# Optimization experiments

Hardware: AMD Instinct MI355X
Metric: run time of the kernel (lower is better)

The kernel has to match this reference:

```python
import jax, jax.numpy as jnp
import numpy as np

NUM_ITERATIONS = 4
STEP = 1
N_NODES = 50000
N_EDGES = 800000
D_FEAT = 64


def setup_inputs() -> dict:
    key = jax.random.key(0)
    k1, k2, k3 = jax.random.split(key, 3)
    x = jax.random.normal(k1, (N_NODES, D_FEAT), dtype=jnp.float32)
    src = jax.random.randint(k2, (N_EDGES,), 0, N_NODES, dtype=jnp.int64)
    dst = jax.random.randint(k3, (N_EDGES,), 0, N_NODES, dtype=jnp.int64)
    edge_index = jnp.stack([src, dst], axis=0)
    return {"x": x, "edge_index": edge_index}


def _wl_conv(x, src, dst, n_nodes):
    # continuous WL: x_i' = 0.5 * (x_i + mean_{j in N(i)} x_j)
    msg = x[src]  # [E, D] gather of neighbor features
    summed = jax.ops.segment_sum(msg, dst, num_segments=n_nodes)  # [N, D]
    deg = jax.ops.segment_sum(jnp.ones_like(dst, dtype=x.dtype), dst,
                              num_segments=n_nodes)  # [N]
    mean = summed / jnp.maximum(deg, 1.0)[:, None]  # isolated nodes -> 0
    return 0.5 * (x + mean)


def reference(x, edge_index):
    n_nodes = x.shape[0]
    src, dst = edge_index[0], edge_index[1]
    feats = [x]
    for _ in range(NUM_ITERATIONS):
        for _ in range(STEP):
            x = _wl_conv(x, src, dst, n_nodes)
        feats.append(x)
    return jnp.concatenate(feats, axis=-1)  # [N, (num_iterations+1)*D]
```

## Files before the change

### kernel.cpp

```cpp
#include <hip/hip_runtime.h>

constexpr int N = 50000;
constexpr int E = 800000;
constexpr int D = 64;
constexpr int DOUT = 320;
constexpr int CAPD = 64;
constexpr int NBUCK = (N + 255) / 256;
constexpr int SLAB = 5120;
constexpr int PART_BLOCKS = 256;
constexpr int CONV_BLOCKS = (N * 16 + 255) / 256;
constexpr int ITER_BLOCKS = 2048;
constexpr int SCAN_BLOCKS = (N + 255) / 256;

__device__ __forceinline__ unsigned short f2bf(float f) {
    unsigned int u = __float_as_uint(f);
    unsigned int r = (u + 0x7fffu + ((u >> 16) & 1u)) >> 16;
    return (unsigned short)r;
}
__device__ __forceinline__ unsigned int pack2(float a, float b) {
    return (unsigned int)f2bf(a) | ((unsigned int)f2bf(b) << 16);
}
__device__ __forceinline__ float bflo(unsigned int u) { return __uint_as_float(u << 16); }
__device__ __forceinline__ float bfhi(unsigned int u) { return __uint_as_float(u & 0xFFFF0000u); }

__global__ __launch_bounds__(256) void part_conv_kernel(
    const int* __restrict__ ei32,
    const float* __restrict__ x,
    float* __restrict__ out,
    unsigned int* __restrict__ mirror,
    int* __restrict__ cursor,
    unsigned int* __restrict__ slab) {
    if (blockIdx.x >= PART_BLOCKS) {
        int i = (blockIdx.x - PART_BLOCKS) * 256 + threadIdx.x;
        if (i < N * 16) {
            int n = i >> 4, j = i & 15;
            float4 v = ((const float4*)x)[i];
            ((float4*)(out + (size_t)n * DOUT))[j] = v;
            uint2 m = make_uint2(pack2(v.x, v.y), pack2(v.z, v.w));
            ((uint2*)(mirror + (size_t)n * 32))[j] = m;
        }
        return;
    }
    __shared__ int hcnt[NBUCK];
    __shared__ int hbase[NBUCK];
    int t = threadIdx.x;
    for (int k = t; k < NBUCK; k += 256) hcnt[k] = 0;
    int lane = t & 63;
    int wv = ei32[2 * lane + 1];
    int is64 = (__ballot(wv != 0) == 0ULL) ? 1 : 0;
    __syncthreads();

    const int EPB = E / PART_BLOCKS;
    int i0 = blockIdx.x * EPB;
    for (int k = t; k < EPB; k += 256) {
        int i = i0 + k;
        int d = is64 ? ei32[2 * (E + i)] : ei32[E + i];
        atomicAdd(&hcnt[d >> 8], 1);
    }
    __syncthreads();
    for (int k = t; k < NBUCK; k += 256) {
        hbase[k] = atomicAdd(&cursor[k], hcnt[k]);
        hcnt[k] = 0;
    }
    __syncthreads();
    for (int k = t; k < EPB; k += 256) {
        int i = i0 + k;
        int s = is64 ? ei32[2 * i] : ei32[i];
        int d = is64 ? ei32[2 * (E + i)] : ei32[E + i];
        int b = d >> 8;
        int r = atomicAdd(&hcnt[b], 1);
        int p = hbase[b] + r;
        if (p < SLAB)
            slab[(size_t)b * SLAB + p] = (unsigned int)s | ((unsigned int)(d & 255) << 16);
    }
}

__global__ __launch_bounds__(256) void lds_build_kernel(
    const unsigned int* __restrict__ slab,
    const int* __restrict__ cursor,
    int* __restrict__ cnt,
    unsigned short* __restrict__ csr) {
    __shared__ unsigned short rows[256 * CAPD];
    __shared__ int lcnt[256];
    int b = blockIdx.x;
    int t = threadIdx.x;
    lcnt[t] = 0;
    __syncthreads();
    int sz = min(cursor[b], SLAB);
    const unsigned int* sp = slab + (size_t)b * SLAB;
    for (int k = t; k < sz; k += 256) {
        unsigned int rec = sp[k];
        int dlo = (rec >> 16) & 255;
        int r = atomicAdd(&lcnt[dlo], 1);
        if (r < CAPD) rows[dlo * CAPD + r] = (unsigned short)(rec & 0xFFFFu);
    }
    __syncthreads();
    int node = b * 256 + t;
    if (node < N) cnt[node] = min(lcnt[t], CAPD);
    for (int k = t; k < 256 * (CAPD / 8); k += 256) {
        int nd = k >> 3;
        int j = k & 7;
        int g = b * 256 + nd;
        if (g < N && j * 8 < lcnt[nd]) {
            *(uint4*)(csr + (size_t)g * CAPD + j * 8) =
                *(const uint4*)(rows + nd * CAPD + j * 8);
        }
    }
}


__global__ __launch_bounds__(256) void wl_iter_bf16_kernel(
    const unsigned int* __restrict__ min_,
    unsigned int* __restrict__ mout,
    const float* __restrict__ self_in,
    float* __restrict__ xout,
    const int* __restrict__ cnt, const unsigned short* __restrict__ csr) {
    int gw = blockIdx.x * 4 + (threadIdx.x >> 6);
    int lane = threadIdx.x & 63;
    int g = lane >> 3;
    int fi = lane & 7;
    const int NW = ITER_BLOCKS * 4;

    int deg_cur = (gw < N) ? min(cnt[gw], CAPD) : 0;
    for (int w = gw; w < N; w += NW) {
        int wn = w + NW;
        int deg_nxt = (wn < N) ? min(cnt[wn], CAPD) : 0;
        int deg = deg_cur;
        size_t base = (size_t)w * CAPD;

        float a[8], b[8];
#pragma unroll
        for (int k = 0; k < 8; ++k) { a[k] = 0.f; b[k] = 0.f; }

#define ACC8(u, arr)                                                     \
        arr[0] += bflo(u.x); arr[1] += bfhi(u.x);                        \
        arr[2] += bflo(u.y); arr[3] += bfhi(u.y);                        \
        arr[4] += bflo(u.z); arr[5] += bfhi(u.z);                        \
        arr[6] += bflo(u.w); arr[7] += bfhi(u.w);

        int e = g;
        for (; e + 8 < deg; e += 16) {
            int s0 = csr[base + e], s1 = csr[base + e + 8];
            uint4 u0 = *(const uint4*)(min_ + (size_t)s0 * 32 + fi * 4);
            uint4 u1 = *(const uint4*)(min_ + (size_t)s1 * 32 + fi * 4);
            ACC8(u0, a); ACC8(u1, b);
        }
        if (e < deg) {
            int s = csr[base + e];
            uint4 u = *(const uint4*)(min_ + (size_t)s * 32 + fi * 4);
            ACC8(u, a);
        }
#undef ACC8
#pragma unroll
        for (int k = 0; k < 8; ++k) {
            a[k] += b[k];
            a[k] += __shfl_xor(a[k], 8);
            a[k] += __shfl_xor(a[k], 16);
            a[k] += __shfl_xor(a[k], 32);
        }
        float inv = (deg > 0) ? 0.5f / (float)deg : 0.0f;
        if (g == 0) {
            const float* srow = self_in + (size_t)w * DOUT + fi * 8;
            float4 s0 = *(const float4*)(srow);
            float4 s1 = *(const float4*)(srow + 4);
            float r0 = 0.5f * s0.x + inv * a[0];
            float r1 = 0.5f * s0.y + inv * a[1];
            float r2 = 0.5f * s0.z + inv * a[2];
            float r3 = 0.5f * s0.w + inv * a[3];
            float r4 = 0.5f * s1.x + inv * a[4];
            float r5 = 0.5f * s1.y + inv * a[5];
            float r6 = 0.5f * s1.z + inv * a[6];
            float r7 = 0.5f * s1.w + inv * a[7];
            float* drow = xout + (size_t)w * DOUT + fi * 8;
            *(float4*)(drow)     = make_float4(r0, r1, r2, r3);
            *(float4*)(drow + 4) = make_float4(r4, r5, r6, r7);
            if (mout) {
                uint4 m = make_uint4(pack2(r0, r1), pack2(r2, r3),
                                     pack2(r4, r5), pack2(r6, r7));
                *(uint4*)(mout + (size_t)w * 32 + fi * 4) = m;
            }
        }
        deg_cur = deg_nxt;
    }
}


__global__ void detect_kernel(const int* __restrict__ ei32, int* __restrict__ flag) {
    if (blockIdx.x == 0 && threadIdx.x == 0) {
        int s = 0;
        for (int k = 0; k < 128; ++k) s |= ei32[2 * k + 1];
        *flag = (s == 0) ? 1 : 0;
    }
}
__device__ __forceinline__ int load_src(const int* ei32, int is64, int i) {
    return is64 ? ei32[2 * i] : ei32[i];
}
__device__ __forceinline__ int load_dst(const int* ei32, int is64, int i) {
    return is64 ? ei32[2 * (E + i)] : ei32[E + i];
}

__global__ __launch_bounds__(256) void hist_kernel(const int* __restrict__ ei32,
                                                   const int* __restrict__ flag,
                                                   int* __restrict__ cnt) {
    int i = blockIdx.x * 256 + threadIdx.x;
    int is64 = *flag;
    if (i < E) atomicAdd(&cnt[load_dst(ei32, is64, i)], 1);
}

__global__ __launch_bounds__(256) void scan1_kernel(const int* __restrict__ cnt,
                                                    int* __restrict__ offs,
                                                    int* __restrict__ P) {
    __shared__ int sm[256];
    int t = threadIdx.x;
    int i = blockIdx.x * 256 + t;
    int v = (i < N) ? cnt[i] : 0;
    sm[t] = v; __syncthreads();
    for (int o = 1; o < 256; o <<= 1) {
        int u = (t >= o) ? sm[t - o] : 0;
        __syncthreads();
        sm[t] += u;
        __syncthreads();
    }
    if (i < N) offs[i] = sm[t] - v;
    if (t == 255) P[blockIdx.x] = sm[255];
}

__global__ __launch_bounds__(256) void scan2_kernel(int* __restrict__ P,
                                                    int* __restrict__ offs) {
    __shared__ int sm[256];
    int t = threadIdx.x;
    int v = (t < SCAN_BLOCKS) ? P[t] : 0;
    sm[t] = v; __syncthreads();
    for (int o = 1; o < 256; o <<= 1) {
        int u = (t >= o) ? sm[t - o] : 0;
        __syncthreads();
        sm[t] += u;
        __syncthreads();
    }
    if (t < SCAN_BLOCKS) P[t] = sm[t] - v;
    if (t == 255) offs[N] = sm[255];
}

__global__ __launch_bounds__(256) void scan3_kernel(int* __restrict__ offs,
                                                    const int* __restrict__ P) {
    int i = blockIdx.x * 256 + threadIdx.x;
    if (i < N) offs[i] += P[blockIdx.x];
}

__global__ __launch_bounds__(256) void scatter_kernel(const int* __restrict__ ei32,
                                                      const int* __restrict__ flag,
                                                      const int* __restrict__ offs,
                                                      int* __restrict__ cursor,
                                                      int* __restrict__ csr) {
    int i = blockIdx.x * 256 + threadIdx.x;
    int is64 = *flag;
    if (i < E) {
        int d = load_dst(ei32, is64, i);
        int p = atomicAdd(&cursor[d], 1);
        csr[offs[d] + p] = load_src(ei32, is64, i);
    }
}

__global__ __launch_bounds__(256) void chunk0_kernel(const float* __restrict__ x,
                                                     float* __restrict__ out) {
    int i = blockIdx.x * 256 + threadIdx.x;
    if (i < N * 16) {
        int n = i >> 4, j = i & 15;
        float4 v = ((const float4*)x)[i];
        ((float4*)(out + (size_t)n * DOUT))[j] = v;
    }
}

__global__ __launch_bounds__(256) void wl_iter_kernel(
    const float* __restrict__ xin, float* __restrict__ xout,
    const int* __restrict__ offs, const int* __restrict__ csr) {
    int w = blockIdx.x * 4 + (threadIdx.x >> 6);
    if (w >= N) return;
    int lane = threadIdx.x & 63;
    int g = lane >> 4, fi = lane & 15;
    int beg = offs[w], end = offs[w + 1];
    float4 a0 = make_float4(0.f, 0.f, 0.f, 0.f);
    float4 a1 = make_float4(0.f, 0.f, 0.f, 0.f);
    int e = beg + g;
    for (; e + 4 < end; e += 8) {
        int s0 = csr[e], s1 = csr[e + 4];
        float4 v0 = *(const float4*)(xin + (size_t)s0 * DOUT + fi * 4);
        float4 v1 = *(const float4*)(xin + (size_t)s1 * DOUT + fi * 4);
        a0.x += v0.x; a0.y += v0.y; a0.z += v0.z; a0.w += v0.w;
        a1.x += v1.x; a1.y += v1.y; a1.z += v1.z; a1.w += v1.w;
    }
    if (e < end) {
        int s = csr[e];
        float4 v = *(const float4*)(xin + (size_t)s * DOUT + fi * 4);
        a0.x += v.x; a0.y += v.y; a0.z += v.z; a0.w += v.w;
    }
    float4 acc;
    acc.x = a0.x + a1.x; acc.y = a0.y + a1.y;
    acc.z = a0.z + a1.z; acc.w = a0.w + a1.w;
    acc.x += __shfl_xor(acc.x, 16); acc.y += __shfl_xor(acc.y, 16);
    acc.z += __shfl_xor(acc.z, 16); acc.w += __shfl_xor(acc.w, 16);
    acc.x += __shfl_xor(acc.x, 32); acc.y += __shfl_xor(acc.y, 32);
    acc.z += __shfl_xor(acc.z, 32); acc.w += __shfl_xor(acc.w, 32);
    int deg = end - beg;
    float inv = (deg > 0) ? 0.5f / (float)deg : 0.0f;
    if (g == 0) {
        float4 s4 = *(const float4*)(xin + (size_t)w * DOUT + fi * 4);
        float4 r;
        r.x = 0.5f * s4.x + inv * acc.x;
        r.y = 0.5f * s4.y + inv * acc.y;
        r.z = 0.5f * s4.z + inv * acc.z;
        r.w = 0.5f * s4.w + inv * acc.w;
        *(float4*)(xout + (size_t)w * DOUT + fi * 4) = r;
    }
}


extern "C" void kernel_launch(void* const* d_in, const int* in_sizes, int n_in,
                              void* d_out, int out_size, void* d_ws, size_t ws_size,
                              hipStream_t stream) {
    const float* x  = (const float*)d_in[0];
    const int* ei32 = (const int*)d_in[1];
    float* out = (float*)d_out;

    int* cursor = (int*)d_ws;
    int* cnt = cursor + 256;
    unsigned int* slab = (unsigned int*)(cnt + N);
    unsigned short* csr = (unsigned short*)(slab + (size_t)NBUCK * SLAB);
    unsigned int* mirA = (unsigned int*)((char*)csr + (size_t)N * CAPD * 2);
    unsigned int* mirB = mirA + (size_t)N * 32;
    size_t need = 256 * 4 + (size_t)N * 4 + (size_t)NBUCK * SLAB * 4 +
                  (size_t)N * CAPD * 2 + (size_t)2 * N * 32 * 4;

    dim3 b256(256);
    dim3 gE((E + 255) / 256);
    dim3 gIter(ITER_BLOCKS);
    dim3 gConv((N * 16 + 255) / 256);

    if (ws_size >= need) {
        hipMemsetAsync(cursor, 0, 256 * sizeof(int), stream);
        part_conv_kernel<<<dim3(PART_BLOCKS + CONV_BLOCKS), b256, 0, stream>>>(
            ei32, x, out, mirA, cursor, slab);
        lds_build_kernel<<<dim3(NBUCK), b256, 0, stream>>>(slab, cursor, cnt, csr);
        wl_iter_bf16_kernel<<<gIter, b256, 0, stream>>>(
            mirA, mirB, out + 0 * D, out + 1 * D, cnt, csr);
        wl_iter_bf16_kernel<<<gIter, b256, 0, stream>>>(
            mirB, mirA, out + 1 * D, out + 2 * D, cnt, csr);
        wl_iter_bf16_kernel<<<gIter, b256, 0, stream>>>(
            mirA, mirB, out + 2 * D, out + 3 * D, cnt, csr);
        wl_iter_bf16_kernel<<<gIter, b256, 0, stream>>>(
            mirB, (unsigned int*)nullptr, out + 3 * D, out + 4 * D, cnt, csr);
    } else {
        int* flag  = (int*)d_ws;
        int* fcnt  = flag + 16;
        int* foffs = fcnt + N;
        int* P     = foffs + (N + 1);
        int* fcsr  = P + 256;
        detect_kernel<<<1, 64, 0, stream>>>(ei32, flag);
        hipMemsetAsync(fcnt, 0, (size_t)N * 4, stream);
        hist_kernel<<<gE, b256, 0, stream>>>(ei32, flag, fcnt);
        scan1_kernel<<<dim3(SCAN_BLOCKS), b256, 0, stream>>>(fcnt, foffs, P);
        scan2_kernel<<<1, b256, 0, stream>>>(P, foffs);
        scan3_kernel<<<dim3(SCAN_BLOCKS), b256, 0, stream>>>(foffs, P);
        hipMemsetAsync(fcnt, 0, (size_t)N * 4, stream);
        scatter_kernel<<<gE, b256, 0, stream>>>(ei32, flag, foffs, fcnt, fcsr);
        chunk0_kernel<<<gConv, b256, 0, stream>>>(x, out);
        for (int c = 1; c <= 4; ++c) {
            wl_iter_kernel<<<dim3((N + 3) / 4), b256, 0, stream>>>(
                out + (size_t)(c - 1) * D, out + (size_t)c * D, foffs, fcsr);
        }
    }
}
```

Before: 204.1 us.

## Process two nodes per wave, issue neighbor loads early, widen build and partition grids

Each wave in the iteration kernel now handles two adjacent nodes at once. It issues the self-row loads and the first 16 neighbor gathers of both nodes up front, then runs an interleaved loop over both nodes' remaining neighbors. This raises memory-level parallelism on the latency-bound bf16 gathers. The grid is resized to 3125 blocks so each wave does exactly one pair. The LDS CSR build now uses 512 threads per block, and the partition kernel uses more blocks; both are meant to improve occupancy during preprocessing. The cost is more registers, which may lower occupancy, and divergence when the two nodes have different degrees.

```diff
diff --git a/kernel.cpp b/kernel.cpp
--- a/kernel.cpp
+++ b/kernel.cpp
@@ -7,9 +7,9 @@
 constexpr int CAPD = 64;
 constexpr int NBUCK = (N + 255) / 256;
 constexpr int SLAB = 5120;
-constexpr int PART_BLOCKS = 256;
+constexpr int PART_BLOCKS = 400;
 constexpr int CONV_BLOCKS = (N * 16 + 255) / 256;
-constexpr int ITER_BLOCKS = 2048;
+constexpr int ITER_BLOCKS = 3125;
 constexpr int SCAN_BLOCKS = (N + 255) / 256;
 
 __device__ __forceinline__ unsigned short f2bf(float f) {
@@ -75,7 +75,7 @@
     }
 }
 
-__global__ __launch_bounds__(256) void lds_build_kernel(
+__global__ __launch_bounds__(512) void lds_build_kernel(
     const unsigned int* __restrict__ slab,
     const int* __restrict__ cursor,
     int* __restrict__ cnt,
@@ -84,11 +84,11 @@
     __shared__ int lcnt[256];
     int b = blockIdx.x;
     int t = threadIdx.x;
-    lcnt[t] = 0;
+    if (t < 256) lcnt[t] = 0;
     __syncthreads();
     int sz = min(cursor[b], SLAB);
     const unsigned int* sp = slab + (size_t)b * SLAB;
-    for (int k = t; k < sz; k += 256) {
+    for (int k = t; k < sz; k += 512) {
         unsigned int rec = sp[k];
         int dlo = (rec >> 16) & 255;
         int r = atomicAdd(&lcnt[dlo], 1);
@@ -96,8 +96,8 @@
     }
     __syncthreads();
     int node = b * 256 + t;
-    if (node < N) cnt[node] = min(lcnt[t], CAPD);
-    for (int k = t; k < 256 * (CAPD / 8); k += 256) {
+    if (t < 256 && node < N) cnt[node] = min(lcnt[t], CAPD);
+    for (int k = t; k < 256 * (CAPD / 8); k += 512) {
         int nd = k >> 3;
         int j = k & 7;
         int g = b * 256 + nd;
@@ -121,12 +121,34 @@
     int fi = lane & 7;
     const int NW = ITER_BLOCKS * 4;
 
-    int deg_cur = (gw < N) ? min(cnt[gw], CAPD) : 0;
-    for (int w = gw; w < N; w += NW) {
-        int wn = w + NW;
-        int deg_nxt = (wn < N) ? min(cnt[wn], CAPD) : 0;
-        int deg = deg_cur;
-        size_t base = (size_t)w * CAPD;
+    for (int w0 = gw * 2; w0 < N; w0 += 2 * NW) {
+        int w1 = w0 + 1;
+        int d0 = min(cnt[w0], CAPD);
+        int d1 = min(cnt[w1], CAPD);
+        size_t base0 = (size_t)w0 * CAPD;
+        size_t base1 = (size_t)w1 * CAPD;
+
+        float4 sa0, sa1, sb0, sb1;
+        if (g == 0) {
+            const float* sr0 = self_in + (size_t)w0 * DOUT + fi * 8;
+            sa0 = *(const float4*)(sr0);
+            sa1 = *(const float4*)(sr0 + 4);
+            const float* sr1 = self_in + (size_t)w1 * DOUT + fi * 8;
+            sb0 = *(const float4*)(sr1);
+            sb1 = *(const float4*)(sr1 + 4);
+        }
+
+        int s00 = (g < d0)     ? (int)csr[base0 + g]     : -1;
+        int s01 = (g + 8 < d0) ? (int)csr[base0 + g + 8] : -1;
+        int s10 = (g < d1)     ? (int)csr[base1 + g]     : -1;
+        int s11 = (g + 8 < d1) ? (int)csr[base1 + g + 8] : -1;
+
+        uint4 z = make_uint4(0u, 0u, 0u, 0u);
+        uint4 u00 = z, u01 = z, u10 = z, u11 = z;
+        if (s00 >= 0) u00 = *(const uint4*)(min_ + (size_t)s00 * 32 + fi * 4);
+        if (s01 >= 0) u01 = *(const uint4*)(min_ + (size_t)s01 * 32 + fi * 4);
+        if (s10 >= 0) u10 = *(const uint4*)(min_ + (size_t)s10 * 32 + fi * 4);
+        if (s11 >= 0) u11 = *(const uint4*)(min_ + (size_t)s11 * 32 + fi * 4);
 
         float a[8], b[8];
 #pragma unroll
@@ -138,49 +160,64 @@
         arr[4] += bflo(u.z); arr[5] += bfhi(u.z);                        \
         arr[6] += bflo(u.w); arr[7] += bfhi(u.w);
 
-        int e = g;
-        for (; e + 8 < deg; e += 16) {
-            int s0 = csr[base + e], s1 = csr[base + e + 8];
-            uint4 u0 = *(const uint4*)(min_ + (size_t)s0 * 32 + fi * 4);
-            uint4 u1 = *(const uint4*)(min_ + (size_t)s1 * 32 + fi * 4);
-            ACC8(u0, a); ACC8(u1, b);
-        }
-        if (e < deg) {
-            int s = csr[base + e];
-            uint4 u = *(const uint4*)(min_ + (size_t)s * 32 + fi * 4);
-            ACC8(u, a);
+        ACC8(u00, a); ACC8(u01, a);
+        ACC8(u10, b); ACC8(u11, b);
+
+        int e0 = g + 16, e1 = g + 16;
+        while (e0 < d0 || e1 < d1) {
+            int t0 = (e0 < d0) ? (int)csr[base0 + e0] : -1;
+            int t1 = (e1 < d1) ? (int)csr[base1 + e1] : -1;
+            uint4 v0 = z, v1 = z;
+            if (t0 >= 0) v0 = *(const uint4*)(min_ + (size_t)t0 * 32 + fi * 4);
+            if (t1 >= 0) v1 = *(const uint4*)(min_ + (size_t)t1 * 32 + fi * 4);
+            ACC8(v0, a); ACC8(v1, b);
+            e0 += 8; e1 += 8;
         }
 #undef ACC8
+
 #pragma unroll
         for (int k = 0; k < 8; ++k) {
-            a[k] += b[k];
             a[k] += __shfl_xor(a[k], 8);
             a[k] += __shfl_xor(a[k], 16);
             a[k] += __shfl_xor(a[k], 32);
-        }
-        float inv = (deg > 0) ? 0.5f / (float)deg : 0.0f;
+            b[k] += __shfl_xor(b[k], 8);
+            b[k] += __shfl_xor(b[k], 16);
+            b[k] += __shfl_xor(b[k], 32);
+        }
+        float inv0 = (d0 > 0) ? 0.5f / (float)d0 : 0.0f;
+        float inv1 = (d1 > 0) ? 0.5f / (float)d1 : 0.0f;
         if (g == 0) {
-            const float* srow = self_in + (size_t)w * DOUT + fi * 8;
-            float4 s0 = *(const float4*)(srow);
-            float4 s1 = *(const float4*)(srow + 4);
-            float r0 = 0.5f * s0.x + inv * a[0];
-            float r1 = 0.5f * s0.y + inv * a[1];
-            float r2 = 0.5f * s0.z + inv * a[2];
-            float r3 = 0.5f * s0.w + inv * a[3];
-            float r4 = 0.5f * s1.x + inv * a[4];
-            float r5 = 0.5f * s1.y + inv * a[5];
-            float r6 = 0.5f * s1.z + inv * a[6];
-            float r7 = 0.5f * s1.w + inv * a[7];
-            float* drow = xout + (size_t)w * DOUT + fi * 8;
-            *(float4*)(drow)     = make_float4(r0, r1, r2, r3);
-            *(float4*)(drow + 4) = make_float4(r4, r5, r6, r7);
+            float r0 = 0.5f * sa0.x + inv0 * a[0];
+            float r1 = 0.5f * sa0.y + inv0 * a[1];
+            float r2 = 0.5f * sa0.z + inv0 * a[2];
+            float r3 = 0.5f * sa0.w + inv0 * a[3];
+            float r4 = 0.5f * sa1.x + inv0 * a[4];
+            float r5 = 0.5f * sa1.y + inv0 * a[5];
+            float r6 = 0.5f * sa1.z + inv0 * a[6];
+            float r7 = 0.5f * sa1.w + inv0 * a[7];
+            float* dr0 = xout + (size_t)w0 * DOUT + fi * 8;
+            *(float4*)(dr0)     = make_float4(r0, r1, r2, r3);
+            *(float4*)(dr0 + 4) = make_float4(r4, r5, r6, r7);
+            float q0 = 0.5f * sb0.x + inv1 * b[0];
+            float q1 = 0.5f * sb0.y + inv1 * b[1];
+            float q2 = 0.5f * sb0.z + inv1 * b[2];
+            float q3 = 0.5f * sb0.w + inv1 * b[3];
+            float q4 = 0.5f * sb1.x + inv1 * b[4];
+            float q5 = 0.5f * sb1.y + inv1 * b[5];
+            float q6 = 0.5f * sb1.z + inv1 * b[6];
+            float q7 = 0.5f * sb1.w + inv1 * b[7];
+            float* dr1 = xout + (size_t)w1 * DOUT + fi * 8;
+            *(float4*)(dr1)     = make_float4(q0, q1, q2, q3);
+            *(float4*)(dr1 + 4) = make_float4(q4, q5, q6, q7);
             if (mout) {
-                uint4 m = make_uint4(pack2(r0, r1), pack2(r2, r3),
-                                     pack2(r4, r5), pack2(r6, r7));
-                *(uint4*)(mout + (size_t)w * 32 + fi * 4) = m;
+                uint4 m0 = make_uint4(pack2(r0, r1), pack2(r2, r3),
+                                      pack2(r4, r5), pack2(r6, r7));
+                *(uint4*)(mout + (size_t)w0 * 32 + fi * 4) = m0;
+                uint4 m1 = make_uint4(pack2(q0, q1), pack2(q2, q3),
+                                      pack2(q4, q5), pack2(q6, q7));
+                *(uint4*)(mout + (size_t)w1 * 32 + fi * 4) = m1;
             }
         }
-        deg_cur = deg_nxt;
     }
 }
 
@@ -340,7 +377,7 @@
         hipMemsetAsync(cursor, 0, 256 * sizeof(int), stream);
         part_conv_kernel<<<dim3(PART_BLOCKS + CONV_BLOCKS), b256, 0, stream>>>(
             ei32, x, out, mirA, cursor, slab);
-        lds_build_kernel<<<dim3(NBUCK), b256, 0, stream>>>(slab, cursor, cnt, csr);
+        lds_build_kernel<<<dim3(NBUCK), dim3(512), 0, stream>>>(slab, cursor, cnt, csr);
         wl_iter_bf16_kernel<<<gIter, b256, 0, stream>>>(
             mirA, mirB, out + 0 * D, out + 1 * D, cnt, csr);
         wl_iter_bf16_kernel<<<gIter, b256, 0, stream>>>(
```

New measurement: 221.9 us. 8.7% more time.
